# Optimization experiments

Measured on AMD Instinct MI355X. Metric: run time of the kernel, lower is better.

The kernel has to match this reference:

```python
import jax, jax.numpy as jnp
import numpy as np

N = 50000   # nodes
E = 800000  # edges
G = 64      # graphs in batch
D = 128     # joint_embed_dim
H = D // 2  # 64
NEG_SLOPE = 0.2


def _segment_softmax(logits, seg, n):
    m = jax.ops.segment_max(logits, seg, num_segments=n)
    m = jnp.where(jnp.isfinite(m), m, 0.0)
    e = jnp.exp(logits - m[seg])
    s = jax.ops.segment_sum(e, seg, num_segments=n)
    return e / (s[seg] + 1e-16)


def _gat_conv(x, src, dst, W, a_src, a_dst, b, n):
    # PyG GATConv, heads=1, add_self_loops=True
    loops = jnp.arange(n, dtype=src.dtype)
    s = jnp.concatenate([src, loops])
    d = jnp.concatenate([dst, loops])
    h = x @ W                                   # [n, out]
    alpha_s = h @ a_src                         # [n]
    alpha_d = h @ a_dst
    logit = jax.nn.leaky_relu(alpha_s[s] + alpha_d[d], NEG_SLOPE)  # [E+n]
    alpha = _segment_softmax(logit, d, n)
    out = jax.ops.segment_sum(h[s] * alpha[:, None], d, num_segments=n)
    return out + b


def _edge_conv(x, src, dst, We1, be1, We2, be2, n):
    # PyG EdgeConv: max_j nn(cat[x_i, x_j - x_i])
    xi = x[dst]
    xj = x[src]
    feats = jnp.concatenate([xi, xj - xi], axis=1)     # [E, 2*H]
    m = jax.nn.relu(feats @ We1 + be1)
    m = jax.nn.relu(m @ We2 + be2)
    out = jax.ops.segment_max(m, dst, num_segments=n)
    return jnp.where(jnp.isfinite(out), out, 0.0)


def setup_inputs() -> dict:
    key = jax.random.key(0)
    ks = jax.random.split(key, 24)
    x = jax.random.normal(ks[0], (N, 3), dtype=jnp.float32)
    edge_index = jax.random.randint(ks[1], (2, E), 0, N, dtype=jnp.int64)
    batch_ids = jnp.sort(jax.random.randint(ks[2], (N,), 0, G, dtype=jnp.int64))

    def w(k, shape, fan_in):
        return jax.random.normal(k, shape, dtype=jnp.float32) * (1.0 / np.sqrt(fan_in))

    inp = {
        "x": x, "edge_index": edge_index, "batch_ids": batch_ids,
        # GATConv1: 3 -> 64
        "W1": w(ks[3], (3, H), 3), "a1s": w(ks[4], (H,), H), "a1d": w(ks[5], (H,), H), "b1": jnp.zeros((H,), jnp.float32),
        # GATConv2: 64 -> 64
        "W2": w(ks[6], (H, H), H), "a2s": w(ks[7], (H,), H), "a2d": w(ks[8], (H,), H), "b2": jnp.zeros((H,), jnp.float32),
        # GATConv3: 128 -> 128
        "W3": w(ks[9], (D, D), D), "a3s": w(ks[10], (D,), D), "a3d": w(ks[11], (D,), D), "b3": jnp.zeros((D,), jnp.float32),
        # EdgeConv nn: 128 -> 128 -> 128
        "We1": w(ks[12], (D, D), D), "be1": jnp.zeros((D,), jnp.float32),
        "We2": w(ks[13], (D, D), D), "be2": jnp.zeros((D,), jnp.float32),
        # MLP: 256 -> 128 -> 128
        "Wm1": w(ks[14], (2 * D, D), 2 * D), "bm1": jnp.zeros((D,), jnp.float32),
        "Wm2": w(ks[15], (D, D), D), "bm2": jnp.zeros((D,), jnp.float32),
    }
    return inp


def reference(x, edge_index, batch_ids,
              W1, a1s, a1d, b1, W2, a2s, a2d, b2, W3, a3s, a3d, b3,
              We1, be1, We2, be2, Wm1, bm1, Wm2, bm2):
    src, dst = edge_index[0], edge_index[1]
    n = x.shape[0]
    # conv1 + relu (dropout is identity in eval)
    h = jax.nn.relu(_gat_conv(x, src, dst, W1, a1s, a1d, b1, n))
    # conv2 + elu
    h = jax.nn.elu(_gat_conv(h, src, dst, W2, a2s, a2d, b2, n))
    # edge_conv: 64 -> 128
    h = _edge_conv(h, src, dst, We1, be1, We2, be2, n)
    # conv3 + relu
    h = jax.nn.relu(_gat_conv(h, src, dst, W3, a3s, a3d, b3, n))
    # global mean / max pool over graphs
    sums = jax.ops.segment_sum(h, batch_ids, num_segments=G)
    cnts = jax.ops.segment_sum(jnp.ones((n, 1), h.dtype), batch_ids, num_segments=G)
    mean_pool = sums / jnp.maximum(cnts, 1.0)
    max_pool = jax.ops.segment_max(h, batch_ids, num_segments=G)
    max_pool = jnp.where(jnp.isfinite(max_pool), max_pool, 0.0)
    z = jnp.concatenate([mean_pool, max_pool], axis=1)    # [G, 256]
    z = jax.nn.relu(z @ Wm1 + bm1)
    z = jax.nn.relu(z @ Wm2 + bm2)
    norm = jnp.linalg.norm(z, axis=1, keepdims=True)
    return z / jnp.maximum(norm, 1e-12)
```

## Files before the change

kernel.cpp:

```cpp
#include <hip/hip_runtime.h>
#include <hip/hip_bf16.h>
#include <math.h>


typedef __attribute__((ext_vector_type(4))) float f32x4;
typedef __attribute__((ext_vector_type(8))) short bf16x8;
typedef short s16x2 __attribute__((ext_vector_type(2)));

__device__ __forceinline__ float wave_sum(float v) {
#pragma unroll
  for (int o = 32; o > 0; o >>= 1) v += __shfl_xor(v, o, 64);
  return v;
}
__device__ __forceinline__ float half_sum(float v) {
#pragma unroll
  for (int o = 16; o > 0; o >>= 1) v += __shfl_xor(v, o, 64);
  return v;
}
__device__ __forceinline__ float lrelu(float x) { return x >= 0.f ? x : 0.2f * x; }
__device__ __forceinline__ ushort f2bf(float f) {
  union { float f; unsigned u; } v; v.f = f;
  unsigned r = (v.u + 0x7fff + ((v.u >> 16) & 1)) >> 16;
  return (ushort)r;
}
__device__ __forceinline__ float bflo(unsigned v) { return __uint_as_float(v << 16); }
__device__ __forceinline__ float bfhi(unsigned v) { return __uint_as_float(v & 0xffff0000u); }
__device__ __forceinline__ unsigned pack2bf(float a, float b) {
  __hip_bfloat162 h = __float22bfloat162_rn(make_float2(a, b));
  union { __hip_bfloat162 h; unsigned u; } cv;
  cv.h = h;
  return cv.u;
}
__device__ __forceinline__ unsigned bfadd2_relu(unsigned a, unsigned b) {
  union { unsigned u; __hip_bfloat162 h; s16x2 s; } ua, ub, ur;
  ua.u = a;
  ub.u = b;
  ur.h = __hadd2(ua.h, ub.h);
  s16x2 z = (s16x2)0;
  ur.s = __builtin_elementwise_max(ur.s, z);
  return ur.u;
}


__global__ void prep_kernel(const float* __restrict__ We1, const float* __restrict__ We2,
                            const float* __restrict__ W2, const float* __restrict__ W3,
                            const float* __restrict__ a2s, const float* __restrict__ a2d,
                            const float* __restrict__ a3s, const float* __restrict__ a3d,
                            ushort* __restrict__ Wpqcm, ushort* __restrict__ We2cm,
                            ushort* __restrict__ W2cm, ushort* __restrict__ W3cm,
                            float* __restrict__ wa2s, float* __restrict__ wa2d,
                            float* __restrict__ wa3s, float* __restrict__ wa3d,
                            int* __restrict__ deg, float* __restrict__ H3,
                            float* __restrict__ psum2, int n, int G) {
  const int b = blockIdx.x, tid = threadIdx.x;
  if (b < 64) {
    const int i = b * 256 + tid, j = i >> 6, k = i & 63;
    const float v = (j < 128) ? (We1[k * 128 + j] - We1[(64 + k) * 128 + j])
                              : We1[(64 + k) * 128 + (j - 128)];
    Wpqcm[j * 64 + k] = f2bf(v);
  } else if (b < 128) {
    const int i = (b - 64) * 256 + tid, k = i >> 7, c = i & 127;
    We2cm[c * 128 + k] = f2bf(We2[k * 128 + c]);
  } else if (b < 192) {
    const int i = (b - 128) * 256 + tid, k = i >> 7, c = i & 127;
    W3cm[c * 128 + k] = f2bf(W3[k * 128 + c]);
  } else if (b < 208) {
    const int i = (b - 192) * 256 + tid, k = i >> 6, c = i & 63;
    W2cm[c * 64 + k] = f2bf(W2[k * 64 + c]);
  } else if (b == 208) {
    if (tid < 128) {
      float s = 0.f, d = 0.f;
      for (int j = 0; j < 128; ++j) {
        const float w = W3[tid * 128 + j];
        s += w * a3s[j];
        d += w * a3d[j];
      }
      wa3s[tid] = s;
      wa3d[tid] = d;
    }
  } else if (b == 209) {
    if (tid < 64) {
      float s = 0.f, d = 0.f;
      for (int j = 0; j < 64; ++j) {
        const float w = W2[tid * 64 + j];
        s += w * a2s[j];
        d += w * a2d[j];
      }
      wa2s[tid] = s;
      wa2d[tid] = d;
    }
  } else {
    const int gtid = (b - 210) * 256 + tid;
    const int stride = (gridDim.x - 210) * 256;
    for (int i = gtid; i < n; i += stride) deg[i] = 0;
    const uint4 z = {0, 0, 0, 0};
    uint4* H4 = (uint4*)H3;
    for (int i = gtid; i < n * 32; i += stride) H4[i] = z;
    uint4* P4 = (uint4*)psum2;
    for (int i = gtid; i < G * 64; i += stride) P4[i] = z;
  }
}


__global__ void count_kernel(const int* __restrict__ ei, int* __restrict__ deg, int E) {
  int e = blockIdx.x * 256 + threadIdx.x;
  if (e < E) atomicAdd(&deg[ei[E + e]], 1);
}

__global__ void scan_local(const int* __restrict__ deg, int* __restrict__ off,
                           int* __restrict__ bsum, int n) {
  __shared__ int buf[256];
  int i = blockIdx.x * 256 + threadIdx.x;
  int v = (i < n) ? deg[i] : 0;
  buf[threadIdx.x] = v;
  __syncthreads();
  int incl = v;
  for (int o = 1; o < 256; o <<= 1) {
    int t = (threadIdx.x >= o) ? buf[threadIdx.x - o] : 0;
    __syncthreads();
    incl += t;
    buf[threadIdx.x] = incl;
    __syncthreads();
  }
  if (i < n) off[i] = incl - v;
  if (threadIdx.x == 255) bsum[blockIdx.x] = incl;
}

__global__ void scan_bsum(int* __restrict__ bsum, int nb) {
  __shared__ int buf[256];
  int v = (threadIdx.x < nb) ? bsum[threadIdx.x] : 0;
  buf[threadIdx.x] = v;
  __syncthreads();
  int incl = v;
  for (int o = 1; o < 256; o <<= 1) {
    int t = (threadIdx.x >= o) ? buf[threadIdx.x - o] : 0;
    __syncthreads();
    incl += t;
    buf[threadIdx.x] = incl;
    __syncthreads();
  }
  if (threadIdx.x < nb) bsum[threadIdx.x] = incl - v;
}

__global__ void scan_add(int* __restrict__ off, const int* __restrict__ bsum, int n, int total) {
  int i = blockIdx.x * 256 + threadIdx.x;
  if (i < n) off[i] += bsum[blockIdx.x];
  if (i == 0) off[n] = total;
}

__global__ void scatter_kernel(const int* __restrict__ ei, const int* __restrict__ off,
                               int* __restrict__ deg, int* __restrict__ csr_src,
                               int* __restrict__ csr_dst, int E) {
  int e = blockIdx.x * 256 + threadIdx.x;
  if (e < E) {
    int d = ei[E + e];
    int pos = off[d] + atomicSub(&deg[d], 1) - 1;
    csr_src[pos] = ei[e];
    csr_dst[pos] = d;
  }
}


template <int IN, int OUT>
__global__ __launch_bounds__(256) void node_linear_kernel(
    const float* __restrict__ x, const float* __restrict__ W,
    const float* __restrict__ av_s, const float* __restrict__ av_d,
    ushort* __restrict__ hb, float* __restrict__ as_out, float* __restrict__ ad_out, int n) {
  constexpr int NB = 4;
  __shared__ float Wl[IN * OUT];
  for (int i = threadIdx.x; i < IN * OUT; i += 256) Wl[i] = W[i];
  __syncthreads();
  const int wid = threadIdx.x >> 6, lane = threadIdx.x & 63;
  const int n0 = (blockIdx.x * 4 + wid) * NB;
  if (n0 >= n) return;
  float acc[NB];
#pragma unroll
  for (int j = 0; j < NB; ++j) acc[j] = 0.f;
  int nidx[NB];
#pragma unroll
  for (int j = 0; j < NB; ++j) nidx[j] = min(n0 + j, n - 1);

  for (int k = 0; k < IN; ++k) {
    const float w = Wl[k * OUT + lane];
#pragma unroll
    for (int j = 0; j < NB; ++j) acc[j] += x[nidx[j] * IN + k] * w;
  }

  const float a_sv = av_s[lane], a_dv = av_d[lane];
#pragma unroll
  for (int j = 0; j < NB; ++j) {
    int node = n0 + j;
    if (node >= n) break;
    float ps = acc[j] * a_sv, pd = acc[j] * a_dv;
    hb[(size_t)node * OUT + lane] = f2bf(acc[j]);
    ps = wave_sum(ps);
    pd = wave_sum(pd);
    if (lane == 0) {
      as_out[node] = ps;
      ad_out[node] = pd;
    }
  }
}


#define NT 64
#define M1S 136
#define M2S 132

__global__ __launch_bounds__(256, 4) void node_mfma_kernel(
    const float* __restrict__ x, const ushort* __restrict__ Wcm,
    const float* __restrict__ wa_s, const float* __restrict__ wa_d,
    ushort* __restrict__ hb, float* __restrict__ as_out, float* __restrict__ ad_out, int n) {
  __shared__ __align__(16) char smem[NT * M2S * 4];
  __shared__ float swa[128], swd[128];
  ushort* m1 = (ushort*)smem;
  float* m2 = (float*)smem;
  const int tid = threadIdx.x;
  const int lane = tid & 63, wid = tid >> 6;
  const int quad = lane >> 4, l16 = lane & 15;
  const int row = tid >> 2, c0 = (tid & 3) * 32;

  bf16x8 bfrag[2][4];
#pragma unroll
  for (int ct = 0; ct < 2; ++ct) {
    const int nn = wid * 32 + ct * 16 + l16;
#pragma unroll
    for (int ks = 0; ks < 4; ++ks)
      bfrag[ct][ks] = *(const bf16x8*)&Wcm[nn * 128 + ks * 32 + quad * 8];
  }
  if (tid < 128) {
    swa[tid] = wa_s[tid];
    swd[tid] = wa_d[tid];
  }
  __syncthreads();

  const int n0 = blockIdx.x * NT;
  const int node = min(n0 + row, n - 1);

  float ps = 0.f, pd = 0.f;
  {
    const float4* xp = (const float4*)&x[(size_t)node * 128 + c0];
#pragma unroll
    for (int i = 0; i < 4; ++i) {
      const float4 a = xp[2 * i], b = xp[2 * i + 1];
      const float4 wa0 = *(const float4*)&swa[c0 + 8 * i];
      const float4 wa1 = *(const float4*)&swa[c0 + 8 * i + 4];
      const float4 wd0 = *(const float4*)&swd[c0 + 8 * i];
      const float4 wd1 = *(const float4*)&swd[c0 + 8 * i + 4];
      ps += a.x * wa0.x + a.y * wa0.y + a.z * wa0.z + a.w * wa0.w
          + b.x * wa1.x + b.y * wa1.y + b.z * wa1.z + b.w * wa1.w;
      pd += a.x * wd0.x + a.y * wd0.y + a.z * wd0.z + a.w * wd0.w
          + b.x * wd1.x + b.y * wd1.y + b.z * wd1.z + b.w * wd1.w;
      uint4 rr;
      rr.x = pack2bf(a.x, a.y);
      rr.y = pack2bf(a.z, a.w);
      rr.z = pack2bf(b.x, b.y);
      rr.w = pack2bf(b.z, b.w);
      *((uint4*)&m1[row * M1S + c0] + i) = rr;
    }
  }
  ps += __shfl_xor(ps, 1, 64);
  ps += __shfl_xor(ps, 2, 64);
  pd += __shfl_xor(pd, 1, 64);
  pd += __shfl_xor(pd, 2, 64);
  if ((tid & 3) == 0 && n0 + row < n) {
    as_out[n0 + row] = ps;
    ad_out[n0 + row] = pd;
  }
  __syncthreads();

  f32x4 acc[4][2];
#pragma unroll
  for (int rt = 0; rt < 4; ++rt)
#pragma unroll
    for (int ct = 0; ct < 2; ++ct) acc[rt][ct] = (f32x4)0.f;
#pragma unroll
  for (int ks = 0; ks < 4; ++ks) {
    bf16x8 afr[4];
#pragma unroll
    for (int rt = 0; rt < 4; ++rt)
      afr[rt] = *(const bf16x8*)&m1[(rt * 16 + l16) * M1S + ks * 32 + quad * 8];
#pragma unroll
    for (int rt = 0; rt < 4; ++rt)
#pragma unroll
      for (int ct = 0; ct < 2; ++ct)
        acc[rt][ct] = __builtin_amdgcn_mfma_f32_16x16x32_bf16(afr[rt], bfrag[ct][ks],
                                                              acc[rt][ct], 0, 0, 0);
  }
  __syncthreads();

#pragma unroll
  for (int ct = 0; ct < 2; ++ct) {
    const int col = wid * 32 + ct * 16 + l16;
#pragma unroll
    for (int rt = 0; rt < 4; ++rt)
#pragma unroll
      for (int r = 0; r < 4; ++r) {
        const int rr2 = rt * 16 + quad * 4 + r;
        m2[rr2 * M2S + col] = acc[rt][ct][r];
      }
  }
  __syncthreads();

  unsigned* hbu = (unsigned*)hb;
#pragma unroll
  for (int i = 0; i < 16; ++i) {
    const int r = wid + 4 * i;
    if (n0 + r < n)
      hbu[(size_t)(n0 + r) * 64 + lane] =
          pack2bf(m2[r * M2S + 2 * lane], m2[r * M2S + 2 * lane + 1]);
  }
}


#define M1S64 72
#define M2S64 68

__global__ __launch_bounds__(256, 4) void node_mfma64_kernel(
    const float* __restrict__ x, const ushort* __restrict__ Wcm,
    const float* __restrict__ wa_s, const float* __restrict__ wa_d,
    ushort* __restrict__ hb, float* __restrict__ as_out, float* __restrict__ ad_out, int n) {
  __shared__ __align__(16) char smem[NT * M2S64 * 4];
  __shared__ float swa[64], swd[64];
  ushort* m1 = (ushort*)smem;
  float* m2 = (float*)smem;
  const int tid = threadIdx.x;
  const int lane = tid & 63, wid = tid >> 6;
  const int quad = lane >> 4, l16 = lane & 15;
  const int row = tid >> 2, c0 = (tid & 3) * 16;

  bf16x8 bfrag[2];
#pragma unroll
  for (int ks = 0; ks < 2; ++ks)
    bfrag[ks] = *(const bf16x8*)&Wcm[(wid * 16 + l16) * 64 + ks * 32 + quad * 8];
  if (tid < 64) {
    swa[tid] = wa_s[tid];
    swd[tid] = wa_d[tid];
  }
  __syncthreads();

  const int n0 = blockIdx.x * NT;
  const int node = min(n0 + row, n - 1);

  float ps = 0.f, pd = 0.f;
  {
    const float4* xp = (const float4*)&x[(size_t)node * 64 + c0];
#pragma unroll
    for (int i = 0; i < 2; ++i) {
      const float4 a = xp[2 * i], b = xp[2 * i + 1];
      const float4 wa0 = *(const float4*)&swa[c0 + 8 * i];
      const float4 wa1 = *(const float4*)&swa[c0 + 8 * i + 4];
      const float4 wd0 = *(const float4*)&swd[c0 + 8 * i];
      const float4 wd1 = *(const float4*)&swd[c0 + 8 * i + 4];
      ps += a.x * wa0.x + a.y * wa0.y + a.z * wa0.z + a.w * wa0.w
          + b.x * wa1.x + b.y * wa1.y + b.z * wa1.z + b.w * wa1.w;
      pd += a.x * wd0.x + a.y * wd0.y + a.z * wd0.z + a.w * wd0.w
          + b.x * wd1.x + b.y * wd1.y + b.z * wd1.z + b.w * wd1.w;
      uint4 rr;
      rr.x = pack2bf(a.x, a.y);
      rr.y = pack2bf(a.z, a.w);
      rr.z = pack2bf(b.x, b.y);
      rr.w = pack2bf(b.z, b.w);
      *((uint4*)&m1[row * M1S64 + c0] + i) = rr;
    }
  }
  ps += __shfl_xor(ps, 1, 64);
  ps += __shfl_xor(ps, 2, 64);
  pd += __shfl_xor(pd, 1, 64);
  pd += __shfl_xor(pd, 2, 64);
  if ((tid & 3) == 0 && n0 + row < n) {
    as_out[n0 + row] = ps;
    ad_out[n0 + row] = pd;
  }
  __syncthreads();

  f32x4 acc[4];
#pragma unroll
  for (int rt = 0; rt < 4; ++rt) acc[rt] = (f32x4)0.f;
#pragma unroll
  for (int ks = 0; ks < 2; ++ks) {
    bf16x8 afr[4];
#pragma unroll
    for (int rt = 0; rt < 4; ++rt)
      afr[rt] = *(const bf16x8*)&m1[(rt * 16 + l16) * M1S64 + ks * 32 + quad * 8];
#pragma unroll
    for (int rt = 0; rt < 4; ++rt)
      acc[rt] = __builtin_amdgcn_mfma_f32_16x16x32_bf16(afr[rt], bfrag[ks], acc[rt], 0, 0, 0);
  }
  __syncthreads();

  {
    const int col = wid * 16 + l16;
#pragma unroll
    for (int rt = 0; rt < 4; ++rt)
#pragma unroll
      for (int r = 0; r < 4; ++r) {
        const int rr2 = rt * 16 + quad * 4 + r;
        m2[rr2 * M2S64 + col] = acc[rt][r];
      }
  }
  __syncthreads();

  unsigned* hbu = (unsigned*)hb;
#pragma unroll
  for (int i = 0; i < 8; ++i) {
    const int r = wid * 2 + (lane >> 5) + 8 * i;
    const int j = lane & 31;
    if (n0 + r < n)
      hbu[(size_t)(n0 + r) * 32 + j] =
          pack2bf(m2[r * M2S64 + 2 * j], m2[r * M2S64 + 2 * j + 1]);
  }
}


#define MPQ 132

__global__ __launch_bounds__(256) void pq_mfma_kernel(
    const float* __restrict__ x, const ushort* __restrict__ Wpqcm,
    const float* __restrict__ be1, ushort* __restrict__ P, ushort* __restrict__ Q, int n) {
  __shared__ __align__(16) char smem[NT * MPQ * 4];
  __shared__ float sbias[128];
  ushort* m1 = (ushort*)smem;
  float* m2 = (float*)smem;
  const int tid = threadIdx.x;
  const int lane = tid & 63, wid = tid >> 6;
  const int quad = lane >> 4, l16 = lane & 15;
  const int row = tid >> 2, c0 = (tid & 3) * 16;

  bf16x8 bfrag[4][2];
#pragma unroll
  for (int ct = 0; ct < 4; ++ct)
#pragma unroll
    for (int ks = 0; ks < 2; ++ks)
      bfrag[ct][ks] =
          *(const bf16x8*)&Wpqcm[(wid * 64 + ct * 16 + l16) * 64 + ks * 32 + quad * 8];
  if (tid < 128) sbias[tid] = be1[tid];

  const int n0 = blockIdx.x * NT;
  const int node = min(n0 + row, n - 1);
  {
    const float4* xp = (const float4*)&x[(size_t)node * 64 + c0];
#pragma unroll
    for (int i = 0; i < 2; ++i) {
      const float4 a = xp[2 * i], b = xp[2 * i + 1];
      uint4 rr;
      rr.x = pack2bf(a.x, a.y);
      rr.y = pack2bf(a.z, a.w);
      rr.z = pack2bf(b.x, b.y);
      rr.w = pack2bf(b.z, b.w);
      *((uint4*)&m1[row * M1S64 + c0] + i) = rr;
    }
  }
  __syncthreads();

  f32x4 acc[4][4];
#pragma unroll
  for (int rt = 0; rt < 4; ++rt)
#pragma unroll
    for (int ct = 0; ct < 4; ++ct) acc[rt][ct] = (f32x4)0.f;
#pragma unroll
  for (int ks = 0; ks < 2; ++ks) {
    bf16x8 afr[4];
#pragma unroll
    for (int rt = 0; rt < 4; ++rt)
      afr[rt] = *(const bf16x8*)&m1[(rt * 16 + l16) * M1S64 + ks * 32 + quad * 8];
#pragma unroll
    for (int rt = 0; rt < 4; ++rt)
#pragma unroll
      for (int ct = 0; ct < 4; ++ct)
        acc[rt][ct] = __builtin_amdgcn_mfma_f32_16x16x32_bf16(afr[rt], bfrag[ct][ks],
                                                              acc[rt][ct], 0, 0, 0);
  }
  __syncthreads();

  if (wid < 2) {
#pragma unroll
    for (int ct = 0; ct < 4; ++ct) {
      const int col = wid * 64 + ct * 16 + l16;
#pragma unroll
      for (int rt = 0; rt < 4; ++rt)
#pragma unroll
        for (int r = 0; r < 4; ++r)
          m2[(rt * 16 + quad * 4 + r) * MPQ + col] = acc[rt][ct][r];
    }
  }
  __syncthreads();
  {
    unsigned* Pu = (unsigned*)P;
#pragma unroll
    for (int i = 0; i < 16; ++i) {
      const int idx = i * 256 + tid;
      const int rw = idx >> 6, j = idx & 63;
      if (n0 + rw < n)
        Pu[(size_t)(n0 + rw) * 64 + j] = pack2bf(m2[rw * MPQ + 2 * j] + sbias[2 * j],
                                                 m2[rw * MPQ + 2 * j + 1] + sbias[2 * j + 1]);
    }
  }
  __syncthreads();
  if (wid >= 2) {
#pragma unroll
    for (int ct = 0; ct < 4; ++ct) {
      const int col = (wid - 2) * 64 + ct * 16 + l16;
#pragma unroll
      for (int rt = 0; rt < 4; ++rt)
#pragma unroll
        for (int r = 0; r < 4; ++r)
          m2[(rt * 16 + quad * 4 + r) * MPQ + col] = acc[rt][ct][r];
    }
  }
  __syncthreads();
  {
    unsigned* Qu = (unsigned*)Q;
#pragma unroll
    for (int i = 0; i < 16; ++i) {
      const int idx = i * 256 + tid;
      const int rw = idx >> 6, j = idx & 63;
      if (n0 + rw < n)
        Qu[(size_t)(n0 + rw) * 64 + j] =
            pack2bf(m2[rw * MPQ + 2 * j], m2[rw * MPQ + 2 * j + 1]);
    }
  }
}


template <int ACT>
__global__ __launch_bounds__(256) void gat_agg128h_kernel(
    const ushort* __restrict__ h, const float* __restrict__ as_, const float* __restrict__ ad_,
    const float* __restrict__ bias, const int* __restrict__ off, const int* __restrict__ csr_src,
    float* __restrict__ out, int n) {
  __shared__ float wbuf[4][64];
  __shared__ int sbuf[4][64];
  const int wid = threadIdx.x >> 6, lane = threadIdx.x & 63;
  const int half = lane >> 5, sl = lane & 31;
  const int d0 = blockIdx.x * 8 + wid * 2 + half;
  const bool wr = d0 < n;
  const int d = wr ? d0 : (n - 1);
  const int s0 = off[d], s1 = off[d + 1];
  const float ad = ad_[d];
  const float l_self = lrelu(as_[d] + ad);
  const uint2 selfv = *(const uint2*)&h[(size_t)d * 128 + 4 * sl];

  float esum_l = 0.f, acc0 = 0.f, acc1 = 0.f, acc2 = 0.f, acc3 = 0.f;

  for (int base = s0; base < s1; base += 32) {
    const int cnt = min(32, s1 - base);
    const int idx = base + sl;
    float w_l = 0.f;
    int s_l = 0;
    if (idx < s1) {
      s_l = csr_src[idx];
      w_l = __expf(lrelu(as_[s_l] + ad) - l_self);
    }
    sbuf[wid][half * 32 + sl] = s_l;
    wbuf[wid][half * 32 + sl] = w_l;
    esum_l += w_l;
    __threadfence_block();
    int j = 0;
    for (; j + 8 <= cnt; j += 8) {
      float w[8];
      int a[8];
#pragma unroll
      for (int t = 0; t < 8; ++t) {
        w[t] = wbuf[wid][half * 32 + j + t];
        a[t] = sbuf[wid][half * 32 + j + t];
      }
      uint2 v[8];
#pragma unroll
      for (int t = 0; t < 8; ++t) v[t] = *(const uint2*)&h[(size_t)a[t] * 128 + 4 * sl];
#pragma unroll
      for (int t = 0; t < 8; ++t) {
        acc0 += w[t] * bflo(v[t].x);
        acc1 += w[t] * bfhi(v[t].x);
        acc2 += w[t] * bflo(v[t].y);
        acc3 += w[t] * bfhi(v[t].y);
      }
    }
    for (; j < cnt; ++j) {
      const float wj = wbuf[wid][half * 32 + j];
      const int aj = sbuf[wid][half * 32 + j];
      const uint2 v = *(const uint2*)&h[(size_t)aj * 128 + 4 * sl];
      acc0 += wj * bflo(v.x);
      acc1 += wj * bfhi(v.x);
      acc2 += wj * bflo(v.y);
      acc3 += wj * bfhi(v.y);
    }
    __threadfence_block();
  }
  const float esum = half_sum(esum_l) + 1.f;
  acc0 += bflo(selfv.x);
  acc1 += bfhi(selfv.x);
  acc2 += bflo(selfv.y);
  acc3 += bfhi(selfv.y);
  const float inv = 1.f / (esum + 1e-16f);
  float v0 = acc0 * inv + bias[4 * sl];
  float v1 = acc1 * inv + bias[4 * sl + 1];
  float v2 = acc2 * inv + bias[4 * sl + 2];
  float v3 = acc3 * inv + bias[4 * sl + 3];
  if (ACT == 0) {
    v0 = fmaxf(v0, 0.f);
    v1 = fmaxf(v1, 0.f);
    v2 = fmaxf(v2, 0.f);
    v3 = fmaxf(v3, 0.f);
  } else {
    v0 = v0 > 0.f ? v0 : expm1f(v0);
    v1 = v1 > 0.f ? v1 : expm1f(v1);
    v2 = v2 > 0.f ? v2 : expm1f(v2);
    v3 = v3 > 0.f ? v3 : expm1f(v3);
  }
  if (wr) {
    float4 o4;
    o4.x = v0;
    o4.y = v1;
    o4.z = v2;
    o4.w = v3;
    *(float4*)&out[(size_t)d * 128 + 4 * sl] = o4;
  }
}


template <int ACT>
__global__ __launch_bounds__(256) void gat_agg64_kernel(
    const ushort* __restrict__ h, const float* __restrict__ as_, const float* __restrict__ ad_,
    const float* __restrict__ bias, const int* __restrict__ off, const int* __restrict__ csr_src,
    float* __restrict__ out, int n) {
  __shared__ float wbuf[4][64];
  __shared__ int sbuf[4][64];
  const int wid = threadIdx.x >> 6, lane = threadIdx.x & 63;
  const int half = lane >> 5, sl = lane & 31;
  const int d0 = blockIdx.x * 8 + wid * 2 + half;
  const bool wr = d0 < n;
  const int d = wr ? d0 : (n - 1);
  const int s0 = off[d], s1 = off[d + 1];
  const float ad = ad_[d];
  const float l_self = lrelu(as_[d] + ad);
  const unsigned selfv = *(const unsigned*)&h[(size_t)d * 64 + 2 * sl];

  float esum_l = 0.f, acc0 = 0.f, acc1 = 0.f;

  for (int base = s0; base < s1; base += 32) {
    const int cnt = min(32, s1 - base);
    const int idx = base + sl;
    float w_l = 0.f;
    int s_l = 0;
    if (idx < s1) {
      s_l = csr_src[idx];
      w_l = __expf(lrelu(as_[s_l] + ad) - l_self);
    }
    sbuf[wid][half * 32 + sl] = s_l;
    wbuf[wid][half * 32 + sl] = w_l;
    esum_l += w_l;
    __threadfence_block();
    int j = 0;
    for (; j + 8 <= cnt; j += 8) {
      float w[8];
      int a[8];
#pragma unroll
      for (int t = 0; t < 8; ++t) {
        w[t] = wbuf[wid][half * 32 + j + t];
        a[t] = sbuf[wid][half * 32 + j + t];
      }
      unsigned v[8];
#pragma unroll
      for (int t = 0; t < 8; ++t) v[t] = *(const unsigned*)&h[(size_t)a[t] * 64 + 2 * sl];
#pragma unroll
      for (int t = 0; t < 8; ++t) {
        acc0 += w[t] * bflo(v[t]);
        acc1 += w[t] * bfhi(v[t]);
      }
    }
    for (; j < cnt; ++j) {
      const float wj = wbuf[wid][half * 32 + j];
      const int aj = sbuf[wid][half * 32 + j];
      const unsigned v = *(const unsigned*)&h[(size_t)aj * 64 + 2 * sl];
      acc0 += wj * bflo(v);
      acc1 += wj * bfhi(v);
    }
    __threadfence_block();
  }
  const float esum = half_sum(esum_l) + 1.f;
  acc0 += bflo(selfv);
  acc1 += bfhi(selfv);
  const float inv = 1.f / (esum + 1e-16f);
  float v0 = acc0 * inv + bias[2 * sl];
  float v1 = acc1 * inv + bias[2 * sl + 1];
  if (ACT == 0) {
    v0 = fmaxf(v0, 0.f);
    v1 = fmaxf(v1, 0.f);
  } else {
    v0 = v0 > 0.f ? v0 : expm1f(v0);
    v1 = v1 > 0.f ? v1 : expm1f(v1);
  }
  if (wr) *(float2*)&out[(size_t)d * 64 + 2 * sl] = make_float2(v0, v1);
}


#define TE 64
#define M2T 68

__global__ __launch_bounds__(256, 4) void edgeconv_mfma_kernel(
    const int* __restrict__ csr_src, const int* __restrict__ csr_dst,
    const ushort* __restrict__ P, const ushort* __restrict__ Q,
    const ushort* __restrict__ We2cm, const float* __restrict__ be2,
    float* __restrict__ out, int E, int ntiles) {
  __shared__ __align__(16) char smem[128 * M2T * 4];
  __shared__ __align__(16) int didx2[2][TE];
  ushort* m1 = (ushort*)smem;
  float* m2t = (float*)smem;
  const int tid = threadIdx.x;
  const int lane = tid & 63, wid = tid >> 6;
  const int quad = lane >> 4, l16 = lane & 15;
  const int row = tid >> 2;
  const int c0 = (tid & 3) * 32;

  bf16x8 bfrag[2][4];
#pragma unroll
  for (int ct = 0; ct < 2; ++ct) {
    const int nn = wid * 32 + ct * 16 + l16;
#pragma unroll
    for (int ks = 0; ks < 4; ++ks)
      bfrag[ct][ks] = *(const bf16x8*)&We2cm[nn * 128 + ks * 32 + quad * 8];
  }
  const float bcol = be2[tid & 127];

  int t = blockIdx.x;
  if (t >= ntiles) return;

  uint4 pv[4], qv[4];
  {
    const int p = t * TE + row;
    int dd = 0, ss = 0;
    if (p < E) { dd = csr_dst[p]; ss = csr_src[p]; }
    const uint4* Pp = (const uint4*)&P[(size_t)dd * 128 + c0];
    const uint4* Qp = (const uint4*)&Q[(size_t)ss * 128 + c0];
#pragma unroll
    for (int i = 0; i < 4; ++i) { pv[i] = Pp[i]; qv[i] = Qp[i]; }
  }
  if (tid < TE) {
    const int p = t * TE + tid;
    didx2[0][tid] = (p < E) ? csr_dst[p] : -1;
  }

  int buf = 0;
  for (; t < ntiles; t += gridDim.x, buf ^= 1) {
    __syncthreads();

#pragma unroll
    for (int i = 0; i < 4; ++i) {
      uint4 rr;
      rr.x = bfadd2_relu(pv[i].x, qv[i].x);
      rr.y = bfadd2_relu(pv[i].y, qv[i].y);
      rr.z = bfadd2_relu(pv[i].z, qv[i].z);
      rr.w = bfadd2_relu(pv[i].w, qv[i].w);
      *((uint4*)&m1[row * M1S + c0] + i) = rr;
    }

    const int tn = t + gridDim.x;
    const bool hasNext = (tn < ntiles);
    int ddn = 0, ssn = 0;
    if (hasNext) {
      const int p = tn * TE + row;
      if (p < E) { ddn = csr_dst[p]; ssn = csr_src[p]; }
      if (tid < TE) {
        const int p2 = tn * TE + tid;
        didx2[buf ^ 1][tid] = (p2 < E) ? csr_dst[p2] : -1;
      }
    }
    __syncthreads();

    f32x4 acc[4][2];
#pragma unroll
    for (int rt = 0; rt < 4; ++rt)
#pragma unroll
      for (int ct = 0; ct < 2; ++ct) acc[rt][ct] = (f32x4)0.f;
#pragma unroll
    for (int ks = 0; ks < 4; ++ks) {
      bf16x8 afr[4];
#pragma unroll
      for (int rt = 0; rt < 4; ++rt)
        afr[rt] = *(const bf16x8*)&m1[(rt * 16 + l16) * M1S + ks * 32 + quad * 8];
#pragma unroll
      for (int rt = 0; rt < 4; ++rt)
#pragma unroll
        for (int ct = 0; ct < 2; ++ct)
          acc[rt][ct] = __builtin_amdgcn_mfma_f32_16x16x32_bf16(afr[rt], bfrag[ct][ks],
                                                                acc[rt][ct], 0, 0, 0);
    }

    if (hasNext) {
      const uint4* Pp = (const uint4*)&P[(size_t)ddn * 128 + c0];
      const uint4* Qp = (const uint4*)&Q[(size_t)ssn * 128 + c0];
#pragma unroll
      for (int i = 0; i < 4; ++i) { pv[i] = Pp[i]; qv[i] = Qp[i]; }
    }
    __syncthreads();

#pragma unroll
    for (int ct = 0; ct < 2; ++ct) {
      const int col = wid * 32 + ct * 16 + l16;
#pragma unroll
      for (int rt = 0; rt < 4; ++rt) {
        float4 mv;
        mv.x = acc[rt][ct][0];
        mv.y = acc[rt][ct][1];
        mv.z = acc[rt][ct][2];
        mv.w = acc[rt][ct][3];
        *(float4*)&m2t[col * M2T + rt * 16 + quad * 4] = mv;
      }
    }
    __syncthreads();

    {
      const int col = tid & 127;
      const int r0 = (tid >> 7) * 32;
      float runmax = -3.0e38f;
      int cur = -2;
      auto flush = [&]() {
        if (cur >= 0)
          atomicMax((int*)&out[(size_t)cur * 128 + col],
                    __float_as_int(fmaxf(runmax + bcol, 0.f)));
      };
#pragma unroll
      for (int i = 0; i < 8; ++i) {
        const int4 dv = *(const int4*)&didx2[buf][r0 + 4 * i];
        const float4 mv = *(const float4*)&m2t[col * M2T + r0 + 4 * i];
        if (dv.x == dv.w) {
          if (dv.x != cur) {
            flush();
            cur = dv.x;
            runmax = -3.0e38f;
          }
          runmax = fmaxf(runmax, fmaxf(fmaxf(mv.x, mv.y), fmaxf(mv.z, mv.w)));
        } else {
          const int da[4] = {dv.x, dv.y, dv.z, dv.w};
          const float ma[4] = {mv.x, mv.y, mv.z, mv.w};
#pragma unroll
          for (int r = 0; r < 4; ++r) {
            if (da[r] != cur) {
              flush();
              cur = da[r];
              runmax = -3.0e38f;
            }
            runmax = fmaxf(runmax, ma[r]);
          }
        }
      }
      flush();
    }
  }
}


__global__ __launch_bounds__(256) void pool_part_kernel(
    const float* __restrict__ h, const int* __restrict__ bid,
    float* __restrict__ psum, float* __restrict__ pmax, int n) {
  const int chunk = (n + gridDim.x - 1) / gridDim.x;
  const int start = blockIdx.x * chunk;
  const int end = min(start + chunk, n);
  if (start >= end) return;
  const int c = threadIdx.x & 127, half = threadIdx.x >> 7;
  float sum = 0.f, mx = 0.f;
  int cur = -1;
  for (int i = start + half; i < end; i += 2) {
    const int g = bid[i];
    if (g != cur) {
      if (cur >= 0) {
        atomicAdd(&psum[cur * 128 + c], sum);
        atomicMax((int*)&pmax[cur * 128 + c], __float_as_int(mx));
      }
      cur = g;
      sum = 0.f;
      mx = 0.f;
    }
    const float v = h[(size_t)i * 128 + c];
    sum += v;
    mx = fmaxf(mx, v);
  }
  if (cur >= 0) {
    atomicAdd(&psum[cur * 128 + c], sum);
    atomicMax((int*)&pmax[cur * 128 + c], __float_as_int(mx));
  }
}


__global__ __launch_bounds__(128) void mlp_kernel(
    const float* __restrict__ psum, const float* __restrict__ pmax,
    const int* __restrict__ bid, int n,
    const float* __restrict__ Wm1, const float* __restrict__ bm1,
    const float* __restrict__ Wm2, const float* __restrict__ bm2,
    float* __restrict__ outp) {
  const int g = blockIdx.x;
  const int c = threadIdx.x;
  __shared__ float zin[256], z1[128];
  __shared__ int scnt;
  if (c == 0) {
    int lo = 0, hi = n;
    while (lo < hi) { int mid = (lo + hi) >> 1; if (bid[mid] < g) lo = mid + 1; else hi = mid; }
    const int start = lo;
    lo = start; hi = n;
    while (lo < hi) { int mid = (lo + hi) >> 1; if (bid[mid] < g + 1) lo = mid + 1; else hi = mid; }
    scnt = lo - start;
  }
  __syncthreads();
  const float invc = 1.f / fmaxf((float)scnt, 1.f);
  zin[c] = psum[g * 128 + c] * invc;
  zin[c + 128] = pmax[g * 128 + c];
  __syncthreads();
  float a = bm1[c];
  for (int k = 0; k < 256; ++k) a += zin[k] * Wm1[k * 128 + c];
  a = fmaxf(a, 0.f);
  z1[c] = a;
  __syncthreads();
  float b = bm2[c];
  for (int k = 0; k < 128; ++k) b += z1[k] * Wm2[k * 128 + c];
  b = fmaxf(b, 0.f);
  float ss = wave_sum(b * b);
  __shared__ float sred[2];
  if ((threadIdx.x & 63) == 0) sred[threadIdx.x >> 6] = ss;
  __syncthreads();
  const float nrm = sqrtf(sred[0] + sred[1]);
  outp[g * 128 + c] = b / fmaxf(nrm, 1e-12f);
}


extern "C" void kernel_launch(void* const* d_in, const int* in_sizes, int n_in, void* d_out,
                              int out_size, void* d_ws, size_t ws_size, hipStream_t stream) {
  const float* x = (const float*)d_in[0];
  const int* ei = (const int*)d_in[1];
  const int* bid = (const int*)d_in[2];
  const float* W1 = (const float*)d_in[3];
  const float* a1s = (const float*)d_in[4];
  const float* a1d = (const float*)d_in[5];
  const float* b1 = (const float*)d_in[6];
  const float* W2 = (const float*)d_in[7];
  const float* a2s = (const float*)d_in[8];
  const float* a2d = (const float*)d_in[9];
  const float* b2 = (const float*)d_in[10];
  const float* W3 = (const float*)d_in[11];
  const float* a3s = (const float*)d_in[12];
  const float* a3d = (const float*)d_in[13];
  const float* b3 = (const float*)d_in[14];
  const float* We1 = (const float*)d_in[15];
  const float* be1 = (const float*)d_in[16];
  const float* We2 = (const float*)d_in[17];
  const float* be2 = (const float*)d_in[18];
  const float* Wm1 = (const float*)d_in[19];
  const float* bm1 = (const float*)d_in[20];
  const float* Wm2 = (const float*)d_in[21];
  const float* bm2v = (const float*)d_in[22];

  const int n = in_sizes[0] / 3;
  const int E = in_sizes[1] / 2;
  const int G = out_size / 128;

  char* w = (char*)d_ws;
  size_t o = 0;
  auto alloc = [&](size_t bytes) {
    void* p = w + o;
    o = (o + bytes + 255) & ~(size_t)255;
    return p;
  };
  int* deg = (int*)alloc((size_t)n * 4);
  int* off = (int*)alloc((size_t)(n + 1) * 4);
  int* bsum = (int*)alloc(1024 * 4);
  int* csr_src = (int*)alloc((size_t)E * 4);
  int* csr_dst = (int*)alloc((size_t)E * 4);
  ushort* We2cm = (ushort*)alloc(128 * 128 * 2);
  ushort* W3cm = (ushort*)alloc(128 * 128 * 2);
  ushort* W2cm = (ushort*)alloc(64 * 64 * 2);
  ushort* Wpqcm = (ushort*)alloc(256 * 64 * 2);
  float* wa3s = (float*)alloc(128 * 4);
  float* wa3d = (float*)alloc(128 * 4);
  float* wa2s = (float*)alloc(64 * 4);
  float* wa2d = (float*)alloc(64 * 4);
  float* as_ = (float*)alloc((size_t)n * 4);
  float* ad_ = (float*)alloc((size_t)n * 4);
  ushort* T64 = (ushort*)alloc((size_t)n * 64 * 2);
  float* X64 = (float*)alloc((size_t)n * 64 * 4);
  ushort* Pbf = (ushort*)alloc((size_t)n * 128 * 2);
  ushort* Qbf = (ushort*)alloc((size_t)n * 128 * 2);
  float* H3 = (float*)alloc((size_t)n * 128 * 4);
  float* psum = (float*)alloc((size_t)G * 128 * 4);
  float* pmax = (float*)alloc((size_t)G * 128 * 4);
  (void)ws_size;

  ushort* Hbf = Pbf;
  float* C3out = H3;

  const int nb256 = (n + 255) / 256;
  const int ebl = (E + 255) / 256;
  const int nlb = (n + 15) / 16;
  const int agb8 = (n + 7) / 8;
  const int ecb = (E + TE - 1) / TE;
  const int nmb = (n + NT - 1) / NT;

  prep_kernel<<<1024, 256, 0, stream>>>(We1, We2, W2, W3, a2s, a2d, a3s, a3d, Wpqcm, We2cm,
                                        W2cm, W3cm, wa2s, wa2d, wa3s, wa3d, deg, H3, psum, n, G);
  count_kernel<<<ebl, 256, 0, stream>>>(ei, deg, E);
  scan_local<<<nb256, 256, 0, stream>>>(deg, off, bsum, n);
  scan_bsum<<<1, 256, 0, stream>>>(bsum, nb256);
  scan_add<<<nb256, 256, 0, stream>>>(off, bsum, n, E);
  scatter_kernel<<<ebl, 256, 0, stream>>>(ei, off, deg, csr_src, csr_dst, E);

  node_linear_kernel<3, 64><<<nlb, 256, 0, stream>>>(x, W1, a1s, a1d, T64, as_, ad_, n);
  gat_agg64_kernel<0><<<agb8, 256, 0, stream>>>(T64, as_, ad_, b1, off, csr_src, X64, n);
  node_mfma64_kernel<<<nmb, 256, 0, stream>>>(X64, W2cm, wa2s, wa2d, T64, as_, ad_, n);
  gat_agg64_kernel<1><<<agb8, 256, 0, stream>>>(T64, as_, ad_, b2, off, csr_src, X64, n);
  pq_mfma_kernel<<<nmb, 256, 0, stream>>>(X64, Wpqcm, be1, Pbf, Qbf, n);
  edgeconv_mfma_kernel<<<1024, 256, 0, stream>>>(csr_src, csr_dst, Pbf, Qbf, We2cm, be2, H3,
                                                 E, ecb);
  node_mfma_kernel<<<nmb, 256, 0, stream>>>(H3, W3cm, wa3s, wa3d, Hbf, as_, ad_, n);
  gat_agg128h_kernel<0><<<agb8, 256, 0, stream>>>(Hbf, as_, ad_, b3, off, csr_src, C3out, n);
  pool_part_kernel<<<512, 256, 0, stream>>>(C3out, bid, psum, pmax, n);
  mlp_kernel<<<G, 128, 0, stream>>>(psum, pmax, bid, n, Wm1, bm1, Wm2, bm2v, (float*)d_out);
}
```

Measured before the change: 429.4 us.

## Use quarter-wave per node in GAT aggregation and bf16 edgeconv staging

The GAT aggregation kernels now assign 16 lanes per destination node instead of 32, so each wave handles four nodes and each lane loads wider vectors (uint4 for 128-dim, uint2 for 64-dim). The edgeconv kernel stages the second MLP output in LDS as bf16 instead of fp32, which halves shared memory so more blocks fit, and its grid is doubled to 2048 blocks. The segment-max pass now reads 8 rows per step. This aims to cut lane underuse on low-degree nodes and LDS pressure, at the cost of an extra bf16 rounding before the max and more serial edge iterations per lane.

Result: no change. 431.5 us (+0.5%).

```diff
diff --git a/kernel.cpp b/kernel.cpp
--- a/kernel.cpp
+++ b/kernel.cpp
@@ -12,9 +12,9 @@
   for (int o = 32; o > 0; o >>= 1) v += __shfl_xor(v, o, 64);
   return v;
 }
-__device__ __forceinline__ float half_sum(float v) {
-#pragma unroll
-  for (int o = 16; o > 0; o >>= 1) v += __shfl_xor(v, o, 64);
+__device__ __forceinline__ float quarter_sum(float v) {
+#pragma unroll
+  for (int o = 8; o > 0; o >>= 1) v += __shfl_xor(v, o, 64);
   return v;
 }
 __device__ __forceinline__ float lrelu(float x) { return x >= 0.f ? x : 0.2f * x; }
@@ -531,28 +531,130 @@
   __shared__ float wbuf[4][64];
   __shared__ int sbuf[4][64];
   const int wid = threadIdx.x >> 6, lane = threadIdx.x & 63;
-  const int half = lane >> 5, sl = lane & 31;
-  const int d0 = blockIdx.x * 8 + wid * 2 + half;
+  const int qid = lane >> 4, ql = lane & 15;
+  const int d0 = blockIdx.x * 16 + wid * 4 + qid;
   const bool wr = d0 < n;
   const int d = wr ? d0 : (n - 1);
   const int s0 = off[d], s1 = off[d + 1];
   const float ad = ad_[d];
   const float l_self = lrelu(as_[d] + ad);
-  const uint2 selfv = *(const uint2*)&h[(size_t)d * 128 + 4 * sl];
-
-  float esum_l = 0.f, acc0 = 0.f, acc1 = 0.f, acc2 = 0.f, acc3 = 0.f;
-
-  for (int base = s0; base < s1; base += 32) {
-    const int cnt = min(32, s1 - base);
-    const int idx = base + sl;
+  const uint4 selfv = *(const uint4*)&h[(size_t)d * 128 + 8 * ql];
+
+  float esum_l = 0.f;
+  float acc[8];
+#pragma unroll
+  for (int c = 0; c < 8; ++c) acc[c] = 0.f;
+
+  for (int base = s0; base < s1; base += 16) {
+    const int cnt = min(16, s1 - base);
+    const int idx = base + ql;
     float w_l = 0.f;
     int s_l = 0;
     if (idx < s1) {
       s_l = csr_src[idx];
       w_l = __expf(lrelu(as_[s_l] + ad) - l_self);
     }
-    sbuf[wid][half * 32 + sl] = s_l;
-    wbuf[wid][half * 32 + sl] = w_l;
+    sbuf[wid][qid * 16 + ql] = s_l;
+    wbuf[wid][qid * 16 + ql] = w_l;
+    esum_l += w_l;
+    __threadfence_block();
+    int j = 0;
+    for (; j + 4 <= cnt; j += 4) {
+      float w[4];
+      int a[4];
+#pragma unroll
+      for (int t = 0; t < 4; ++t) {
+        w[t] = wbuf[wid][qid * 16 + j + t];
+        a[t] = sbuf[wid][qid * 16 + j + t];
+      }
+      uint4 v[4];
+#pragma unroll
+      for (int t = 0; t < 4; ++t) v[t] = *(const uint4*)&h[(size_t)a[t] * 128 + 8 * ql];
+#pragma unroll
+      for (int t = 0; t < 4; ++t) {
+        acc[0] += w[t] * bflo(v[t].x);
+        acc[1] += w[t] * bfhi(v[t].x);
+        acc[2] += w[t] * bflo(v[t].y);
+        acc[3] += w[t] * bfhi(v[t].y);
+        acc[4] += w[t] * bflo(v[t].z);
+        acc[5] += w[t] * bfhi(v[t].z);
+        acc[6] += w[t] * bflo(v[t].w);
+        acc[7] += w[t] * bfhi(v[t].w);
+      }
+    }
+    for (; j < cnt; ++j) {
+      const float wj = wbuf[wid][qid * 16 + j];
+      const int aj = sbuf[wid][qid * 16 + j];
+      const uint4 v = *(const uint4*)&h[(size_t)aj * 128 + 8 * ql];
+      acc[0] += wj * bflo(v.x);
+      acc[1] += wj * bfhi(v.x);
+      acc[2] += wj * bflo(v.y);
+      acc[3] += wj * bfhi(v.y);
+      acc[4] += wj * bflo(v.z);
+      acc[5] += wj * bfhi(v.z);
+      acc[6] += wj * bflo(v.w);
+      acc[7] += wj * bfhi(v.w);
+    }
+    __threadfence_block();
+  }
+  const float esum = quarter_sum(esum_l) + 1.f;
+  acc[0] += bflo(selfv.x);
+  acc[1] += bfhi(selfv.x);
+  acc[2] += bflo(selfv.y);
+  acc[3] += bfhi(selfv.y);
+  acc[4] += bflo(selfv.z);
+  acc[5] += bfhi(selfv.z);
+  acc[6] += bflo(selfv.w);
+  acc[7] += bfhi(selfv.w);
+  const float inv = 1.f / (esum + 1e-16f);
+  float v[8];
+#pragma unroll
+  for (int c = 0; c < 8; ++c) {
+    v[c] = acc[c] * inv + bias[8 * ql + c];
+    if (ACT == 0)
+      v[c] = fmaxf(v[c], 0.f);
+    else
+      v[c] = v[c] > 0.f ? v[c] : expm1f(v[c]);
+  }
+  if (wr) {
+    float4 o0 = {v[0], v[1], v[2], v[3]};
+    float4 o1 = {v[4], v[5], v[6], v[7]};
+    *(float4*)&out[(size_t)d * 128 + 8 * ql] = o0;
+    *(float4*)&out[(size_t)d * 128 + 8 * ql + 4] = o1;
+  }
+}
+
+
+template <int ACT>
+__global__ __launch_bounds__(256) void gat_agg64_kernel(
+    const ushort* __restrict__ h, const float* __restrict__ as_, const float* __restrict__ ad_,
+    const float* __restrict__ bias, const int* __restrict__ off, const int* __restrict__ csr_src,
+    float* __restrict__ out, int n) {
+  __shared__ float wbuf[4][64];
+  __shared__ int sbuf[4][64];
+  const int wid = threadIdx.x >> 6, lane = threadIdx.x & 63;
+  const int qid = lane >> 4, ql = lane & 15;
+  const int d0 = blockIdx.x * 16 + wid * 4 + qid;
+  const bool wr = d0 < n;
+  const int d = wr ? d0 : (n - 1);
+  const int s0 = off[d], s1 = off[d + 1];
+  const float ad = ad_[d];
+  const float l_self = lrelu(as_[d] + ad);
+  const uint2 selfv = *(const uint2*)&h[(size_t)d * 64 + 4 * ql];
+
+  float esum_l = 0.f, acc0 = 0.f, acc1 = 0.f, acc2 = 0.f, acc3 = 0.f;
+
+  for (int base = s0; base < s1; base += 16) {
+    const int cnt = min(16, s1 - base);
+    const int idx = base + ql;
+    float w_l = 0.f;
+    int s_l = 0;
+    if (idx < s1) {
+      s_l = csr_src[idx];
+      w_l = __expf(lrelu(as_[s_l] + ad) - l_self);
+    }
+    sbuf[wid][qid * 16 + ql] = s_l;
+    wbuf[wid][qid * 16 + ql] = w_l;
     esum_l += w_l;
     __threadfence_block();
     int j = 0;
@@ -561,12 +663,12 @@
       int a[8];
 #pragma unroll
       for (int t = 0; t < 8; ++t) {
-        w[t] = wbuf[wid][half * 32 + j + t];
-        a[t] = sbuf[wid][half * 32 + j + t];
+        w[t] = wbuf[wid][qid * 16 + j + t];
+        a[t] = sbuf[wid][qid * 16 + j + t];
       }
       uint2 v[8];
 #pragma unroll
-      for (int t = 0; t < 8; ++t) v[t] = *(const uint2*)&h[(size_t)a[t] * 128 + 4 * sl];
+      for (int t = 0; t < 8; ++t) v[t] = *(const uint2*)&h[(size_t)a[t] * 64 + 4 * ql];
 #pragma unroll
       for (int t = 0; t < 8; ++t) {
         acc0 += w[t] * bflo(v[t].x);
@@ -576,9 +678,9 @@
       }
     }
     for (; j < cnt; ++j) {
-      const float wj = wbuf[wid][half * 32 + j];
-      const int aj = sbuf[wid][half * 32 + j];
-      const uint2 v = *(const uint2*)&h[(size_t)aj * 128 + 4 * sl];
+      const float wj = wbuf[wid][qid * 16 + j];
+      const int aj = sbuf[wid][qid * 16 + j];
+      const uint2 v = *(const uint2*)&h[(size_t)aj * 64 + 4 * ql];
       acc0 += wj * bflo(v.x);
       acc1 += wj * bfhi(v.x);
       acc2 += wj * bflo(v.y);
@@ -586,16 +688,16 @@
     }
     __threadfence_block();
   }
-  const float esum = half_sum(esum_l) + 1.f;
+  const float esum = quarter_sum(esum_l) + 1.f;
   acc0 += bflo(selfv.x);
   acc1 += bfhi(selfv.x);
   acc2 += bflo(selfv.y);
   acc3 += bfhi(selfv.y);
   const float inv = 1.f / (esum + 1e-16f);
-  float v0 = acc0 * inv + bias[4 * sl];
-  float v1 = acc1 * inv + bias[4 * sl + 1];
-  float v2 = acc2 * inv + bias[4 * sl + 2];
-  float v3 = acc3 * inv + bias[4 * sl + 3];
+  float v0 = acc0 * inv + bias[4 * ql];
+  float v1 = acc1 * inv + bias[4 * ql + 1];
+  float v2 = acc2 * inv + bias[4 * ql + 2];
+  float v3 = acc3 * inv + bias[4 * ql + 3];
   if (ACT == 0) {
     v0 = fmaxf(v0, 0.f);
     v1 = fmaxf(v1, 0.f);
@@ -608,104 +710,24 @@
     v3 = v3 > 0.f ? v3 : expm1f(v3);
   }
   if (wr) {
-    float4 o4;
-    o4.x = v0;
-    o4.y = v1;
-    o4.z = v2;
-    o4.w = v3;
-    *(float4*)&out[(size_t)d * 128 + 4 * sl] = o4;
-  }
-}
-
-
-template <int ACT>
-__global__ __launch_bounds__(256) void gat_agg64_kernel(
-    const ushort* __restrict__ h, const float* __restrict__ as_, const float* __restrict__ ad_,
-    const float* __restrict__ bias, const int* __restrict__ off, const int* __restrict__ csr_src,
-    float* __restrict__ out, int n) {
-  __shared__ float wbuf[4][64];
-  __shared__ int sbuf[4][64];
-  const int wid = threadIdx.x >> 6, lane = threadIdx.x & 63;
-  const int half = lane >> 5, sl = lane & 31;
-  const int d0 = blockIdx.x * 8 + wid * 2 + half;
-  const bool wr = d0 < n;
-  const int d = wr ? d0 : (n - 1);
-  const int s0 = off[d], s1 = off[d + 1];
-  const float ad = ad_[d];
-  const float l_self = lrelu(as_[d] + ad);
-  const unsigned selfv = *(const unsigned*)&h[(size_t)d * 64 + 2 * sl];
-
-  float esum_l = 0.f, acc0 = 0.f, acc1 = 0.f;
-
-  for (int base = s0; base < s1; base += 32) {
-    const int cnt = min(32, s1 - base);
-    const int idx = base + sl;
-    float w_l = 0.f;
-    int s_l = 0;
-    if (idx < s1) {
-      s_l = csr_src[idx];
-      w_l = __expf(lrelu(as_[s_l] + ad) - l_self);
-    }
-    sbuf[wid][half * 32 + sl] = s_l;
-    wbuf[wid][half * 32 + sl] = w_l;
-    esum_l += w_l;
-    __threadfence_block();
-    int j = 0;
-    for (; j + 8 <= cnt; j += 8) {
-      float w[8];
-      int a[8];
-#pragma unroll
-      for (int t = 0; t < 8; ++t) {
-        w[t] = wbuf[wid][half * 32 + j + t];
-        a[t] = sbuf[wid][half * 32 + j + t];
-      }
-      unsigned v[8];
-#pragma unroll
-      for (int t = 0; t < 8; ++t) v[t] = *(const unsigned*)&h[(size_t)a[t] * 64 + 2 * sl];
-#pragma unroll
-      for (int t = 0; t < 8; ++t) {
-        acc0 += w[t] * bflo(v[t]);
-        acc1 += w[t] * bfhi(v[t]);
-      }
-    }
-    for (; j < cnt; ++j) {
-      const float wj = wbuf[wid][half * 32 + j];
-      const int aj = sbuf[wid][half * 32 + j];
-      const unsigned v = *(const unsigned*)&h[(size_t)aj * 64 + 2 * sl];
-      acc0 += wj * bflo(v);
-      acc1 += wj * bfhi(v);
-    }
-    __threadfence_block();
-  }
-  const float esum = half_sum(esum_l) + 1.f;
-  acc0 += bflo(selfv);
-  acc1 += bfhi(selfv);
-  const float inv = 1.f / (esum + 1e-16f);
-  float v0 = acc0 * inv + bias[2 * sl];
-  float v1 = acc1 * inv + bias[2 * sl + 1];
-  if (ACT == 0) {
-    v0 = fmaxf(v0, 0.f);
-    v1 = fmaxf(v1, 0.f);
-  } else {
-    v0 = v0 > 0.f ? v0 : expm1f(v0);
-    v1 = v1 > 0.f ? v1 : expm1f(v1);
-  }
-  if (wr) *(float2*)&out[(size_t)d * 64 + 2 * sl] = make_float2(v0, v1);
+    float4 o4 = {v0, v1, v2, v3};
+    *(float4*)&out[(size_t)d * 64 + 4 * ql] = o4;
+  }
 }
 
 
 #define TE 64
-#define M2T 68
+#define M2TB 72
 
 __global__ __launch_bounds__(256, 4) void edgeconv_mfma_kernel(
     const int* __restrict__ csr_src, const int* __restrict__ csr_dst,
     const ushort* __restrict__ P, const ushort* __restrict__ Q,
     const ushort* __restrict__ We2cm, const float* __restrict__ be2,
     float* __restrict__ out, int E, int ntiles) {
-  __shared__ __align__(16) char smem[128 * M2T * 4];
+  __shared__ __align__(16) char smem[128 * M2TB * 2];
   __shared__ __align__(16) int didx2[2][TE];
   ushort* m1 = (ushort*)smem;
-  float* m2t = (float*)smem;
+  ushort* m2t = (ushort*)smem;
   const int tid = threadIdx.x;
   const int lane = tid & 63, wid = tid >> 6;
   const int quad = lane >> 4, l16 = lane & 15;
@@ -799,12 +821,10 @@
       const int col = wid * 32 + ct * 16 + l16;
 #pragma unroll
       for (int rt = 0; rt < 4; ++rt) {
-        float4 mv;
-        mv.x = acc[rt][ct][0];
-        mv.y = acc[rt][ct][1];
-        mv.z = acc[rt][ct][2];
-        mv.w = acc[rt][ct][3];
-        *(float4*)&m2t[col * M2T + rt * 16 + quad * 4] = mv;
+        uint2 mv;
+        mv.x = pack2bf(acc[rt][ct][0], acc[rt][ct][1]);
+        mv.y = pack2bf(acc[rt][ct][2], acc[rt][ct][3]);
+        *(uint2*)&m2t[col * M2TB + rt * 16 + quad * 4] = mv;
       }
     }
     __syncthreads();
@@ -820,21 +840,25 @@
                     __float_as_int(fmaxf(runmax + bcol, 0.f)));
       };
 #pragma unroll
-      for (int i = 0; i < 8; ++i) {
-        const int4 dv = *(const int4*)&didx2[buf][r0 + 4 * i];
-        const float4 mv = *(const float4*)&m2t[col * M2T + r0 + 4 * i];
-        if (dv.x == dv.w) {
-          if (dv.x != cur) {
+      for (int i = 0; i < 4; ++i) {
+        const int4 dv0 = *(const int4*)&didx2[buf][r0 + 8 * i];
+        const int4 dv1 = *(const int4*)&didx2[buf][r0 + 8 * i + 4];
+        const uint4 mv = *(const uint4*)&m2t[col * M2TB + r0 + 8 * i];
+        const float ma[8] = {bflo(mv.x), bfhi(mv.x), bflo(mv.y), bfhi(mv.y),
+                             bflo(mv.z), bfhi(mv.z), bflo(mv.w), bfhi(mv.w)};
+        if (dv0.x == dv1.w) {
+          if (dv0.x != cur) {
             flush();
-            cur = dv.x;
+            cur = dv0.x;
             runmax = -3.0e38f;
           }
-          runmax = fmaxf(runmax, fmaxf(fmaxf(mv.x, mv.y), fmaxf(mv.z, mv.w)));
+          const float m01 = fmaxf(ma[0], ma[1]), m23 = fmaxf(ma[2], ma[3]);
+          const float m45 = fmaxf(ma[4], ma[5]), m67 = fmaxf(ma[6], ma[7]);
+          runmax = fmaxf(runmax, fmaxf(fmaxf(m01, m23), fmaxf(m45, m67)));
         } else {
-          const int da[4] = {dv.x, dv.y, dv.z, dv.w};
-          const float ma[4] = {mv.x, mv.y, mv.z, mv.w};
-#pragma unroll
-          for (int r = 0; r < 4; ++r) {
+          const int da[8] = {dv0.x, dv0.y, dv0.z, dv0.w, dv1.x, dv1.y, dv1.z, dv1.w};
+#pragma unroll
+          for (int r = 0; r < 8; ++r) {
             if (da[r] != cur) {
               flush();
               cur = da[r];
@@ -989,7 +1013,7 @@
   const int nb256 = (n + 255) / 256;
   const int ebl = (E + 255) / 256;
   const int nlb = (n + 15) / 16;
-  const int agb8 = (n + 7) / 8;
+  const int agb16 = (n + 15) / 16;
   const int ecb = (E + TE - 1) / TE;
   const int nmb = (n + NT - 1) / NT;
 
@@ -1002,14 +1026,14 @@
   scatter_kernel<<<ebl, 256, 0, stream>>>(ei, off, deg, csr_src, csr_dst, E);
 
   node_linear_kernel<3, 64><<<nlb, 256, 0, stream>>>(x, W1, a1s, a1d, T64, as_, ad_, n);
-  gat_agg64_kernel<0><<<agb8, 256, 0, stream>>>(T64, as_, ad_, b1, off, csr_src, X64, n);
+  gat_agg64_kernel<0><<<agb16, 256, 0, stream>>>(T64, as_, ad_, b1, off, csr_src, X64, n);
   node_mfma64_kernel<<<nmb, 256, 0, stream>>>(X64, W2cm, wa2s, wa2d, T64, as_, ad_, n);
-  gat_agg64_kernel<1><<<agb8, 256, 0, stream>>>(T64, as_, ad_, b2, off, csr_src, X64, n);
+  gat_agg64_kernel<1><<<agb16, 256, 0, stream>>>(T64, as_, ad_, b2, off, csr_src, X64, n);
   pq_mfma_kernel<<<nmb, 256, 0, stream>>>(X64, Wpqcm, be1, Pbf, Qbf, n);
-  edgeconv_mfma_kernel<<<1024, 256, 0, stream>>>(csr_src, csr_dst, Pbf, Qbf, We2cm, be2, H3,
+  edgeconv_mfma_kernel<<<2048, 256, 0, stream>>>(csr_src, csr_dst, Pbf, Qbf, We2cm, be2, H3,
                                                  E, ecb);
   node_mfma_kernel<<<nmb, 256, 0, stream>>>(H3, W3cm, wa3s, wa3d, Hbf, as_, ad_, n);
-  gat_agg128h_kernel<0><<<agb8, 256, 0, stream>>>(Hbf, as_, ad_, b3, off, csr_src, C3out, n);
+  gat_agg128h_kernel<0><<<agb16, 256, 0, stream>>>(Hbf, as_, ad_, b3, off, csr_src, C3out, n);
   pool_part_kernel<<<512, 256, 0, stream>>>(C3out, bid, psum, pmax, n);
   mlp_kernel<<<G, 128, 0, stream>>>(psum, pmax, bid, n, Wm1, bm1, Wm2, bm2v, (float*)d_out);
 }
```
